# Kernel optimization log

Measured on AMD Instinct MI355X. Metric: run time of the kernel, lower is better.

## Reference

```python
import jax, jax.numpy as jnp
import numpy as np

N_QUBITS = 4
N_LAYERS = 3
B = 65536
EPS = 1e-5  # BatchNorm1d default eps

CNOT = jnp.array([[1, 0, 0, 0],
                  [0, 1, 0, 0],
                  [0, 0, 0, 1],
                  [0, 0, 1, 0]], dtype=jnp.complex64)


def _apply_1q(state, U, q):
    # state: [B, 2,2,2,2]; U: [2,2] (shared) or [B,2,2] (per-sample)
    s = jnp.moveaxis(state, 1 + q, -1)
    if U.ndim == 3:
        s = jnp.einsum('b...j,bij->b...i', s, U)
    else:
        s = jnp.einsum('...j,ij->...i', s, U)
    return jnp.moveaxis(s, -1, 1 + q)


def _apply_cnot(state, c, t):
    s = jnp.moveaxis(state, (1 + c, 1 + t), (-2, -1))
    shp = s.shape
    s = jnp.einsum('...j,ij->...i', s.reshape(shp[:-2] + (4,)), CNOT)
    return jnp.moveaxis(s.reshape(shp), (-2, -1), (1 + c, 1 + t))


def _rx_batched(theta):  # theta: [B] -> [B,2,2]
    c = jnp.cos(theta / 2).astype(jnp.complex64)
    s = (-1j * jnp.sin(theta / 2).astype(jnp.complex64))
    return jnp.stack([jnp.stack([c, s], -1), jnp.stack([s, c], -1)], -2)


def _ry(theta):  # scalar -> [2,2]
    c = jnp.cos(theta / 2).astype(jnp.complex64)
    s = jnp.sin(theta / 2).astype(jnp.complex64)
    return jnp.stack([jnp.stack([c, -s]), jnp.stack([s, c])])


def _rz(theta):  # scalar -> [2,2] diagonal
    e = jnp.exp(-1j * theta.astype(jnp.complex64) / 2)
    z = jnp.zeros_like(e)
    return jnp.stack([jnp.stack([e, z]), jnp.stack([z, jnp.conj(e)])])


def _circuit(angles, qparams):
    bsz = angles.shape[0]
    state = jnp.zeros((bsz, 2 ** N_QUBITS), jnp.complex64).at[:, 0].set(1.0)
    state = state.reshape((bsz,) + (2,) * N_QUBITS)
    for q in range(N_QUBITS):
        state = _apply_1q(state, _rx_batched(angles[:, q]), q)
    for l in range(N_LAYERS):
        for q in range(N_QUBITS):
            state = _apply_1q(state, _ry(qparams[l, q, 0]), q)
            state = _apply_1q(state, _rz(qparams[l, q, 1]), q)
        for q in range(N_QUBITS - 1):
            state = _apply_cnot(state, q, q + 1)
        state = _apply_cnot(state, N_QUBITS - 1, 0)
    probs = jnp.abs(state) ** 2  # [B,2,2,2,2]
    zs = []
    for q in range(N_QUBITS):
        axes = tuple(a for a in range(1, N_QUBITS + 1) if a != 1 + q)
        p = probs.sum(axes)  # [B,2]
        zs.append(p[:, 0] - p[:, 1])
    return jnp.stack(zs, -1)  # [B, n_qubits]


def setup_inputs() -> dict:
    key = jax.random.key(0)
    k1, k2, k3 = jax.random.split(key, 3)
    x = jax.random.normal(k1, (B, 1, 24, 24), dtype=jnp.float32)
    enc_w = 0.1 * jax.random.normal(k2, (N_QUBITS, 16), dtype=jnp.float32)
    enc_b = jnp.zeros((N_QUBITS,), jnp.float32)
    qparams = 0.01 * jax.random.normal(k3, (N_LAYERS, N_QUBITS, 3), dtype=jnp.float32)
    gamma = jnp.ones((N_QUBITS,), jnp.float32)
    beta = jnp.zeros((N_QUBITS,), jnp.float32)
    return {"x": x, "enc_w": enc_w, "enc_b": enc_b, "qparams": qparams,
            "gamma": gamma, "beta": beta}


def reference(x, enc_w, enc_b, qparams, gamma, beta):
    bsz = x.shape[0]
    # avg_pool2d(kernel=6, stride=6): [B,1,24,24] -> [B,1,4,4] -> [B,16]
    pooled = x.reshape(bsz, 1, 4, 6, 4, 6).mean((3, 5)).reshape(bsz, 16)
    angles = pooled @ enc_w.T + enc_b  # [B, n_qubits]
    out = _circuit(angles, qparams)    # [B, n_qubits]
    # BatchNorm1d (training mode: batch stats, biased var)
    mean = out.mean(0)
    var = out.var(0)
    return (out - mean) / jnp.sqrt(var + EPS) * gamma + beta
```

## Files before the change

kernel.cpp:

```cpp
#include <hip/hip_runtime.h>
#include <math.h>


#define BATCH 65536
#define SPW 8
#define MAIN_BLOCKS (BATCH / (4 * SPW))

__global__ __launch_bounds__(256) void qnat_precompute(const float* __restrict__ qp,
                                                       float* __restrict__ A,
                                                       double* __restrict__ acc) {
  __shared__ float Ur[16][17], Ui[16][17];
  const int tid = threadIdx.x;
  if (tid >= 64 && tid < 72) acc[tid - 64] = 0.0;
  if (tid < 16) {
    const int col = tid;
    float ur[16], ui[16];
#pragma unroll
    for (int i = 0; i < 16; i++) { ur[i] = (i == col) ? 1.f : 0.f; ui[i] = 0.f; }
#pragma unroll
    for (int l = 0; l < 3; l++) {
#pragma unroll
      for (int q = 0; q < 4; q++) {
        const int b = 3 - q;
        const float ty = qp[(l * 4 + q) * 3 + 0];
        const float tz = qp[(l * 4 + q) * 3 + 1];
        const float cy = cosf(0.5f * ty), sy = sinf(0.5f * ty);
#pragma unroll
        for (int i0 = 0; i0 < 16; i0++) {
          if (((i0 >> b) & 1) == 0) {
            const int i1 = i0 | (1 << b);
            const float r0 = ur[i0], m0 = ui[i0], r1 = ur[i1], m1 = ui[i1];
            ur[i0] = cy * r0 - sy * r1;  ui[i0] = cy * m0 - sy * m1;
            ur[i1] = sy * r0 + cy * r1;  ui[i1] = sy * m0 + cy * m1;
          }
        }
        const float cz = cosf(0.5f * tz), sz = sinf(0.5f * tz);
#pragma unroll
        for (int i0 = 0; i0 < 16; i0++) {
          if (((i0 >> b) & 1) == 0) {
            const int i1 = i0 | (1 << b);
            const float r0 = ur[i0], m0 = ui[i0], r1 = ur[i1], m1 = ui[i1];
            ur[i0] = cz * r0 + sz * m0;  ui[i0] = cz * m0 - sz * r0;
            ur[i1] = cz * r1 - sz * m1;  ui[i1] = cz * m1 + sz * r1;
          }
        }
      }
      const int cb[4] = {3, 2, 1, 0};
      const int tb[4] = {2, 1, 0, 3};
#pragma unroll
      for (int e = 0; e < 4; e++) {
#pragma unroll
        for (int i = 0; i < 16; i++) {
          if (((i >> cb[e]) & 1) && (((i >> tb[e]) & 1) == 0)) {
            const int j2 = i | (1 << tb[e]);
            float t0 = ur[i]; ur[i] = ur[j2]; ur[j2] = t0;
            float t1 = ui[i]; ui[i] = ui[j2]; ui[j2] = t1;
          }
        }
      }
    }
#pragma unroll
    for (int i = 0; i < 16; i++) { Ur[i][col] = ur[i]; Ui[i][col] = ui[i]; }
  }
  __syncthreads();
  const int j = tid >> 4, k = tid & 15;
#pragma unroll
  for (int q = 0; q < 4; q++) {
    const int b = 3 - q;
    float mr = 0.f, mi = 0.f;
#pragma unroll
    for (int i = 0; i < 16; i++) {
      const float z = ((i >> b) & 1) ? -1.f : 1.f;
      const float ar = Ur[i][j], ai = Ui[i][j], br = Ur[i][k], bi = Ui[i][k];
      mr += z * (ar * br + ai * bi);
      mi += z * (ar * bi - ai * br);
    }
    const int e = (__popc((unsigned)j) - __popc((unsigned)k)) & 3;
    const float re = (e == 0) ? mr : (e == 1) ? -mi : (e == 2) ? -mr : mi;
    A[(q << 8) + tid] = re;
  }
}

__global__ __launch_bounds__(256, 4) void qnat_main(const float* __restrict__ x,
                                                    const float* __restrict__ enc_w,
                                                    const float* __restrict__ enc_b,
                                                    const float* __restrict__ A,
                                                    float* __restrict__ out,
                                                    double* __restrict__ acc) {
  __shared__ float4 sW4[16];
  __shared__ double sAcc[4][4][2];
  const int tid = threadIdx.x;
  if (tid < 16) {
    const float inv36 = 1.0f / 36.0f;
    sW4[tid] = make_float4(enc_w[tid] * inv36, enc_w[16 + tid] * inv36,
                           enc_w[32 + tid] * inv36, enc_w[48 + tid] * inv36);
  }
  __syncthreads();

  const int wave = tid >> 6, lane = tid & 63;
  const int j = lane & 15;
  const int g = lane >> 4;
  const bool bit0 = lane & 1, bit1 = lane & 2;

  float4 wXr[3], wYr[3];
#pragma unroll
  for (int t = 0; t < 3; t++) {
    int p0 = t * 256 + 4 * lane;
    if (p0 > 572) p0 = 572;
    const int row = p0 / 24, col = p0 - row * 24;
    const int rr = (row / 6) * 4;
    wXr[t] = sW4[rr + col / 6];
    wYr[t] = sW4[rr + (col + 3) / 6];
  }
  float Areg[16];
#pragma unroll
  for (int k = 0; k < 16; k++) Areg[k] = A[(g << 8) + (j << 4) + k];
  const float bq = enc_b[lane & 3];

  const int s0 = (blockIdx.x * 4 + wave) * SPW;
  double sd = 0.0, ssd = 0.0;

#define LOADS(S, V0, V1, V2)                                              \
  {                                                                       \
    const float4* p4 = (const float4*)(x + (size_t)(S) * 576);            \
    V0 = p4[lane];                                                        \
    V1 = p4[64 + lane];                                                   \
    V2 = (lane < 16) ? p4[128 + lane] : make_float4(0.f, 0.f, 0.f, 0.f);  \
  }

  float4 xv0, xv1, xv2;
  LOADS(s0, xv0, xv1, xv2);

  for (int i = 0; i < SPW; i++) {
    const int s = s0 + i;
    float4 xn0, xn1, xn2;
    if (i + 1 < SPW) LOADS(s + 1, xn0, xn1, xn2);

    float a0 = 0.f, a1 = 0.f, a2 = 0.f, a3 = 0.f;
#define ACCT(V, T)                                           \
    {                                                        \
      const float h0 = V.x + V.y, h1 = V.z + V.w;            \
      a0 = fmaf(h0, wXr[T].x, fmaf(h1, wYr[T].x, a0));       \
      a1 = fmaf(h0, wXr[T].y, fmaf(h1, wYr[T].y, a1));       \
      a2 = fmaf(h0, wXr[T].z, fmaf(h1, wYr[T].z, a2));       \
      a3 = fmaf(h0, wXr[T].w, fmaf(h1, wYr[T].w, a3));       \
    }
    ACCT(xv0, 0) ACCT(xv1, 1) ACCT(xv2, 2)
#undef ACCT

    float snd, rcv;
    snd = bit0 ? a0 : a1; rcv = __shfl_xor(snd, 1);
    float Af = (bit0 ? a1 : a0) + rcv;
    snd = bit0 ? a2 : a3; rcv = __shfl_xor(snd, 1);
    float Bf = (bit0 ? a3 : a2) + rcv;
    snd = bit1 ? Af : Bf; rcv = __shfl_xor(snd, 2);
    float Cf = (bit1 ? Bf : Af) + rcv;
    Cf += __shfl_xor(Cf, 4);
    Cf += __shfl_xor(Cf, 8);
    Cf += __shfl_xor(Cf, 16);
    Cf += __shfl_xor(Cf, 32);

    float sm, cm;
    __sincosf(0.5f * (Cf + bq), &sm, &cm);

    const int base = lane & ~3;
    const float c0 = __shfl(cm, base + 0), s0_ = __shfl(sm, base + 0);
    const float c1 = __shfl(cm, base + 1), s1_ = __shfl(sm, base + 1);
    const float c2 = __shfl(cm, base + 2), s2_ = __shfl(sm, base + 2);
    const float c3 = __shfl(cm, base + 3), s3_ = __shfl(sm, base + 3);

    const float p01[4] = {c0 * c1, c0 * s1_, s0_ * c1, s0_ * s1_};
    const float p23[4] = {c2 * c3, c2 * s3_, s2_ * c3, s2_ * s3_};
    float inner = 0.f;
#pragma unroll
    for (int hi = 0; hi < 4; hi++) {
      float sh = 0.f;
#pragma unroll
      for (int lo = 0; lo < 4; lo++) sh = fmaf(Areg[4 * hi + lo], p23[lo], sh);
      inner = fmaf(p01[hi], sh, inner);
    }
    const float rj = ((j & 8) ? s0_ : c0) * ((j & 4) ? s1_ : c1) *
                     ((j & 2) ? s2_ : c2) * ((j & 1) ? s3_ : c3);
    float v = inner * rj;
    v += __shfl_xor(v, 1);
    v += __shfl_xor(v, 2);
    v += __shfl_xor(v, 4);
    v += __shfl_xor(v, 8);
    if (j == 0) {
      out[(size_t)s * 4 + g] = v;
      sd += (double)v;
      ssd = fma((double)v, (double)v, ssd);
    }

    if (i + 1 < SPW) { xv0 = xn0; xv1 = xn1; xv2 = xn2; }
  }
#undef LOADS

  if (j == 0) { sAcc[wave][g][0] = sd; sAcc[wave][g][1] = ssd; }
  __syncthreads();
  if (tid < 8) {
    const int q = tid & 3, m = tid >> 2;
    const double t = sAcc[0][q][m] + sAcc[1][q][m] + sAcc[2][q][m] + sAcc[3][q][m];
    atomicAdd(&acc[m * 4 + q], t);
  }
}

__global__ __launch_bounds__(256) void qnat_norm(float* __restrict__ out,
                                                 const double* __restrict__ acc,
                                                 const float* __restrict__ gamma,
                                                 const float* __restrict__ beta) {
  __shared__ float sMean[4], sScale[4], sBeta[4];
  const int tid = threadIdx.x;
  if (tid < 4) {
    const double n = (double)BATCH;
    const double mean = acc[tid] / n;
    const double var = acc[4 + tid] / n - mean * mean;
    const double inv = 1.0 / sqrt(var + 1e-5);
    sMean[tid] = (float)mean;
    sScale[tid] = (float)(gamma[tid] * inv);
    sBeta[tid] = beta[tid];
  }
  __syncthreads();
  const size_t i = (size_t)blockIdx.x * 256 + tid;
  float4 v = ((const float4*)out)[i];
  v.x = (v.x - sMean[0]) * sScale[0] + sBeta[0];
  v.y = (v.y - sMean[1]) * sScale[1] + sBeta[1];
  v.z = (v.z - sMean[2]) * sScale[2] + sBeta[2];
  v.w = (v.w - sMean[3]) * sScale[3] + sBeta[3];
  ((float4*)out)[i] = v;
}

extern "C" void kernel_launch(void* const* d_in, const int* in_sizes, int n_in,
                              void* d_out, int out_size, void* d_ws, size_t ws_size,
                              hipStream_t stream) {
  const float* x       = (const float*)d_in[0];
  const float* enc_w   = (const float*)d_in[1];
  const float* enc_b   = (const float*)d_in[2];
  const float* qparams = (const float*)d_in[3];
  const float* gamma   = (const float*)d_in[4];
  const float* beta    = (const float*)d_in[5];
  float* out = (float*)d_out;

  float* A = (float*)d_ws;
  double* acc = (double*)((char*)d_ws + 4096);

  qnat_precompute<<<1, 256, 0, stream>>>(qparams, A, acc);
  qnat_main<<<MAIN_BLOCKS, 256, 0, stream>>>(x, enc_w, enc_b, A, out, acc);
  qnat_norm<<<256, 256, 0, stream>>>(out, acc, gamma, beta);
}
```

Before: 59.76 us.

## Fuse precompute, main and batchnorm into one kernel with grid barrier

New measurement: 153.6 us. +157.0%, slower.

```diff
diff --git a/kernel.cpp b/kernel.cpp
--- a/kernel.cpp
+++ b/kernel.cpp
@@ -3,15 +3,46 @@
 
 
 #define BATCH 65536
-#define SPW 8
-#define MAIN_BLOCKS (BATCH / (4 * SPW))
-
-__global__ __launch_bounds__(256) void qnat_precompute(const float* __restrict__ qp,
-                                                       float* __restrict__ A,
-                                                       double* __restrict__ acc) {
+#define GRID  512
+#define SPW   32
+
+__global__ __launch_bounds__(256, 4) void qnat_fused(
+    const float* __restrict__ x, const float* __restrict__ enc_w,
+    const float* __restrict__ enc_b, const float* __restrict__ qp,
+    const float* __restrict__ gamma, const float* __restrict__ beta,
+    float* __restrict__ out, double* __restrict__ acc,
+    float* __restrict__ pub, unsigned* __restrict__ bar) {
+
   __shared__ float Ur[16][17], Ui[16][17];
+  __shared__ float sA[4][256];
+  __shared__ float4 sW4[16];
+  __shared__ double sAcc[4][4][2];
+  __shared__ float sNrm[8];
+
   const int tid = threadIdx.x;
-  if (tid >= 64 && tid < 72) acc[tid - 64] = 0.0;
+  const int wave = tid >> 6, lane = tid & 63;
+  const int j = lane & 15;
+  const int g = lane >> 4;
+  const bool bit0 = lane & 1, bit1 = lane & 2;
+  const int s0 = (blockIdx.x * 4 + wave) * SPW;
+
+#define LOADS(S, V0, V1, V2)                                              \
+  {                                                                       \
+    const float4* p4 = (const float4*)(x + (size_t)(S) * 576);            \
+    V0 = p4[lane];                                                        \
+    V1 = p4[64 + lane];                                                   \
+    V2 = (lane < 16) ? p4[128 + lane] : make_float4(0.f, 0.f, 0.f, 0.f);  \
+  }
+
+  float4 xv0, xv1, xv2;
+  LOADS(s0, xv0, xv1, xv2);
+
+  if (tid < 16) {
+    const float inv36 = 1.0f / 36.0f;
+    sW4[tid] = make_float4(enc_w[tid] * inv36, enc_w[16 + tid] * inv36,
+                           enc_w[32 + tid] * inv36, enc_w[48 + tid] * inv36);
+  }
+
   if (tid < 16) {
     const int col = tid;
     float ur[16], ui[16];
@@ -63,44 +94,24 @@
     for (int i = 0; i < 16; i++) { Ur[i][col] = ur[i]; Ui[i][col] = ui[i]; }
   }
   __syncthreads();
-  const int j = tid >> 4, k = tid & 15;
-#pragma unroll
-  for (int q = 0; q < 4; q++) {
-    const int b = 3 - q;
-    float mr = 0.f, mi = 0.f;
-#pragma unroll
-    for (int i = 0; i < 16; i++) {
-      const float z = ((i >> b) & 1) ? -1.f : 1.f;
-      const float ar = Ur[i][j], ai = Ui[i][j], br = Ur[i][k], bi = Ui[i][k];
-      mr += z * (ar * br + ai * bi);
-      mi += z * (ar * bi - ai * br);
-    }
-    const int e = (__popc((unsigned)j) - __popc((unsigned)k)) & 3;
-    const float re = (e == 0) ? mr : (e == 1) ? -mi : (e == 2) ? -mr : mi;
-    A[(q << 8) + tid] = re;
-  }
-}
-
-__global__ __launch_bounds__(256, 4) void qnat_main(const float* __restrict__ x,
-                                                    const float* __restrict__ enc_w,
-                                                    const float* __restrict__ enc_b,
-                                                    const float* __restrict__ A,
-                                                    float* __restrict__ out,
-                                                    double* __restrict__ acc) {
-  __shared__ float4 sW4[16];
-  __shared__ double sAcc[4][4][2];
-  const int tid = threadIdx.x;
-  if (tid < 16) {
-    const float inv36 = 1.0f / 36.0f;
-    sW4[tid] = make_float4(enc_w[tid] * inv36, enc_w[16 + tid] * inv36,
-                           enc_w[32 + tid] * inv36, enc_w[48 + tid] * inv36);
-  }
-  __syncthreads();
-
-  const int wave = tid >> 6, lane = tid & 63;
-  const int j = lane & 15;
-  const int g = lane >> 4;
-  const bool bit0 = lane & 1, bit1 = lane & 2;
+  {
+    const int jj = tid >> 4, kk = tid & 15;
+#pragma unroll
+    for (int q = 0; q < 4; q++) {
+      const int b = 3 - q;
+      float mr = 0.f, mi = 0.f;
+#pragma unroll
+      for (int i = 0; i < 16; i++) {
+        const float z = ((i >> b) & 1) ? -1.f : 1.f;
+        const float ar = Ur[i][jj], ai = Ui[i][jj], br = Ur[i][kk], bi = Ui[i][kk];
+        mr += z * (ar * br + ai * bi);
+        mi += z * (ar * bi - ai * br);
+      }
+      const int e = (__popc((unsigned)jj) - __popc((unsigned)kk)) & 3;
+      sA[q][tid] = (e == 0) ? mr : (e == 1) ? -mi : (e == 2) ? -mr : mi;
+    }
+  }
+  __syncthreads();
 
   float4 wXr[3], wYr[3];
 #pragma unroll
@@ -114,22 +125,10 @@
   }
   float Areg[16];
 #pragma unroll
-  for (int k = 0; k < 16; k++) Areg[k] = A[(g << 8) + (j << 4) + k];
+  for (int k = 0; k < 16; k++) Areg[k] = sA[g][(j << 4) + k];
   const float bq = enc_b[lane & 3];
 
-  const int s0 = (blockIdx.x * 4 + wave) * SPW;
   double sd = 0.0, ssd = 0.0;
-
-#define LOADS(S, V0, V1, V2)                                              \
-  {                                                                       \
-    const float4* p4 = (const float4*)(x + (size_t)(S) * 576);            \
-    V0 = p4[lane];                                                        \
-    V1 = p4[64 + lane];                                                   \
-    V2 = (lane < 16) ? p4[128 + lane] : make_float4(0.f, 0.f, 0.f, 0.f);  \
-  }
-
-  float4 xv0, xv1, xv2;
-  LOADS(s0, xv0, xv1, xv2);
 
   for (int i = 0; i < SPW; i++) {
     const int s = s0 + i;
@@ -203,31 +202,44 @@
     const double t = sAcc[0][q][m] + sAcc[1][q][m] + sAcc[2][q][m] + sAcc[3][q][m];
     atomicAdd(&acc[m * 4 + q], t);
   }
-}
-
-__global__ __launch_bounds__(256) void qnat_norm(float* __restrict__ out,
-                                                 const double* __restrict__ acc,
-                                                 const float* __restrict__ gamma,
-                                                 const float* __restrict__ beta) {
-  __shared__ float sMean[4], sScale[4], sBeta[4];
-  const int tid = threadIdx.x;
-  if (tid < 4) {
-    const double n = (double)BATCH;
-    const double mean = acc[tid] / n;
-    const double var = acc[4 + tid] / n - mean * mean;
-    const double inv = 1.0 / sqrt(var + 1e-5);
-    sMean[tid] = (float)mean;
-    sScale[tid] = (float)(gamma[tid] * inv);
-    sBeta[tid] = beta[tid];
-  }
-  __syncthreads();
-  const size_t i = (size_t)blockIdx.x * 256 + tid;
-  float4 v = ((const float4*)out)[i];
-  v.x = (v.x - sMean[0]) * sScale[0] + sBeta[0];
-  v.y = (v.y - sMean[1]) * sScale[1] + sBeta[1];
-  v.z = (v.z - sMean[2]) * sScale[2] + sBeta[2];
-  v.w = (v.w - sMean[3]) * sScale[3] + sBeta[3];
-  ((float4*)out)[i] = v;
+
+  __syncthreads();
+  if (tid == 0) {
+    __threadfence();
+    const unsigned n = __hip_atomic_fetch_add(bar, 1u, __ATOMIC_ACQ_REL,
+                                              __HIP_MEMORY_SCOPE_AGENT);
+    if (n == GRID - 1) {
+#pragma unroll
+      for (int q = 0; q < 4; q++) {
+        const double s  = __hip_atomic_load(&acc[q],     __ATOMIC_RELAXED, __HIP_MEMORY_SCOPE_AGENT);
+        const double ss = __hip_atomic_load(&acc[4 + q], __ATOMIC_RELAXED, __HIP_MEMORY_SCOPE_AGENT);
+        const double mean = s / (double)BATCH;
+        const double var = ss / (double)BATCH - mean * mean;
+        pub[q] = (float)mean;
+        pub[4 + q] = (float)(1.0 / sqrt(var + 1e-5));
+      }
+      __threadfence();
+      __hip_atomic_store(bar + 1, 1u, __ATOMIC_RELEASE, __HIP_MEMORY_SCOPE_AGENT);
+    }
+    while (__hip_atomic_load(bar + 1, __ATOMIC_ACQUIRE, __HIP_MEMORY_SCOPE_AGENT) == 0u)
+      __builtin_amdgcn_s_sleep(8);
+#pragma unroll
+    for (int i2 = 0; i2 < 8; i2++)
+      sNrm[i2] = __hip_atomic_load(&pub[i2], __ATOMIC_RELAXED, __HIP_MEMORY_SCOPE_AGENT);
+  }
+  __syncthreads();
+
+  {
+    const int q = lane & 3;
+    const float mean = sNrm[q];
+    const float scale = gamma[q] * sNrm[4 + q];
+    const float shift = beta[q];
+    const size_t basee = (size_t)s0 * 4;
+    const float v0 = out[basee + lane];
+    out[basee + lane] = (v0 - mean) * scale + shift;
+    const float v1 = out[basee + 64 + lane];
+    out[basee + 64 + lane] = (v1 - mean) * scale + shift;
+  }
 }
 
 extern "C" void kernel_launch(void* const* d_in, const int* in_sizes, int n_in,
@@ -241,10 +253,11 @@
   const float* beta    = (const float*)d_in[5];
   float* out = (float*)d_out;
 
-  float* A = (float*)d_ws;
-  double* acc = (double*)((char*)d_ws + 4096);
-
-  qnat_precompute<<<1, 256, 0, stream>>>(qparams, A, acc);
-  qnat_main<<<MAIN_BLOCKS, 256, 0, stream>>>(x, enc_w, enc_b, A, out, acc);
-  qnat_norm<<<256, 256, 0, stream>>>(out, acc, gamma, beta);
+  double* acc   = (double*)d_ws;
+  float* pub    = (float*)((char*)d_ws + 64);
+  unsigned* bar = (unsigned*)((char*)d_ws + 96);
+
+  hipMemsetAsync(d_ws, 0, 104, stream);
+  qnat_fused<<<GRID, 256, 0, stream>>>(x, enc_w, enc_b, qparams, gamma, beta,
+                                       out, acc, pub, bar);
 }
```

## Stage input tile into LDS via global_load_lds before per-sample compute

Applied to the files above, without the earlier changes.

Result: slower. 63.88 us (+6.9%).

```diff
diff --git a/kernel.cpp b/kernel.cpp
--- a/kernel.cpp
+++ b/kernel.cpp
@@ -3,8 +3,12 @@
 
 
 #define BATCH 65536
-#define SPW 8
-#define MAIN_BLOCKS (BATCH / (4 * SPW))
+#define SPB 32
+#define MAIN_BLOCKS (BATCH / SPB)
+#define TILE_BYTES (SPB * 576 * 4)
+
+#define AS1C(p) (const __attribute__((address_space(1))) void*)(p)
+#define AS3(p)  (__attribute__((address_space(3))) void*)(p)
 
 __global__ __launch_bounds__(256) void qnat_precompute(const float* __restrict__ qp,
                                                        float* __restrict__ A,
@@ -76,31 +80,48 @@
       mi += z * (ar * bi - ai * br);
     }
     const int e = (__popc((unsigned)j) - __popc((unsigned)k)) & 3;
-    const float re = (e == 0) ? mr : (e == 1) ? -mi : (e == 2) ? -mr : mi;
-    A[(q << 8) + tid] = re;
-  }
-}
-
-__global__ __launch_bounds__(256, 4) void qnat_main(const float* __restrict__ x,
+    A[(q << 8) + tid] = (e == 0) ? mr : (e == 1) ? -mi : (e == 2) ? -mr : mi;
+  }
+}
+
+__global__ __launch_bounds__(256, 2) void qnat_main(const float* __restrict__ x,
                                                     const float* __restrict__ enc_w,
                                                     const float* __restrict__ enc_b,
                                                     const float* __restrict__ A,
                                                     float* __restrict__ out,
                                                     double* __restrict__ acc) {
+  __shared__ float sX[SPB * 576];
   __shared__ float4 sW4[16];
   __shared__ double sAcc[4][4][2];
   const int tid = threadIdx.x;
+  const int wave = tid >> 6, lane = tid & 63;
+
+  {
+    const char* xb = (const char*)x + (size_t)blockIdx.x * TILE_BYTES;
+#pragma unroll
+    for (int i = 0; i < 18; i++) {
+      const int off = (i * 4 + wave) << 10;
+      __builtin_amdgcn_global_load_lds(AS1C(xb + off + lane * 16),
+                                       AS3((char*)sX + off), 16, 0, 0);
+    }
+  }
+
   if (tid < 16) {
     const float inv36 = 1.0f / 36.0f;
     sW4[tid] = make_float4(enc_w[tid] * inv36, enc_w[16 + tid] * inv36,
                            enc_w[32 + tid] * inv36, enc_w[48 + tid] * inv36);
   }
-  __syncthreads();
-
-  const int wave = tid >> 6, lane = tid & 63;
+
   const int j = lane & 15;
   const int g = lane >> 4;
   const bool bit0 = lane & 1, bit1 = lane & 2;
+
+  float Areg[16];
+#pragma unroll
+  for (int k = 0; k < 16; k++) Areg[k] = A[(g << 8) + (j << 4) + k];
+  const float bq = enc_b[lane & 3];
+
+  __syncthreads();
 
   float4 wXr[3], wYr[3];
 #pragma unroll
@@ -112,29 +133,17 @@
     wXr[t] = sW4[rr + col / 6];
     wYr[t] = sW4[rr + (col + 3) / 6];
   }
-  float Areg[16];
-#pragma unroll
-  for (int k = 0; k < 16; k++) Areg[k] = A[(g << 8) + (j << 4) + k];
-  const float bq = enc_b[lane & 3];
-
-  const int s0 = (blockIdx.x * 4 + wave) * SPW;
+
   double sd = 0.0, ssd = 0.0;
 
-#define LOADS(S, V0, V1, V2)                                              \
-  {                                                                       \
-    const float4* p4 = (const float4*)(x + (size_t)(S) * 576);            \
-    V0 = p4[lane];                                                        \
-    V1 = p4[64 + lane];                                                   \
-    V2 = (lane < 16) ? p4[128 + lane] : make_float4(0.f, 0.f, 0.f, 0.f);  \
-  }
-
-  float4 xv0, xv1, xv2;
-  LOADS(s0, xv0, xv1, xv2);
-
-  for (int i = 0; i < SPW; i++) {
-    const int s = s0 + i;
-    float4 xn0, xn1, xn2;
-    if (i + 1 < SPW) LOADS(s + 1, xn0, xn1, xn2);
+#pragma unroll
+  for (int i = 0; i < 8; i++) {
+    const int sl = wave * 8 + i;
+    const int s = blockIdx.x * SPB + sl;
+    const float4* p4 = (const float4*)(sX + sl * 576);
+    const float4 V0 = p4[lane];
+    const float4 V1 = p4[64 + lane];
+    const float4 V2 = (lane < 16) ? p4[128 + lane] : make_float4(0.f, 0.f, 0.f, 0.f);
 
     float a0 = 0.f, a1 = 0.f, a2 = 0.f, a3 = 0.f;
 #define ACCT(V, T)                                           \
@@ -145,7 +154,7 @@
       a2 = fmaf(h0, wXr[T].z, fmaf(h1, wYr[T].z, a2));       \
       a3 = fmaf(h0, wXr[T].w, fmaf(h1, wYr[T].w, a3));       \
     }
-    ACCT(xv0, 0) ACCT(xv1, 1) ACCT(xv2, 2)
+    ACCT(V0, 0) ACCT(V1, 1) ACCT(V2, 2)
 #undef ACCT
 
     float snd, rcv;
@@ -191,10 +200,7 @@
       sd += (double)v;
       ssd = fma((double)v, (double)v, ssd);
     }
-
-    if (i + 1 < SPW) { xv0 = xn0; xv1 = xn1; xv2 = xn2; }
-  }
-#undef LOADS
+  }
 
   if (j == 0) { sAcc[wave][g][0] = sd; sAcc[wave][g][1] = ssd; }
   __syncthreads();
```
